# Performance work log

Hardware: AMD Instinct MI355X
Metric: run time of the kernel (lower is better)

The kernel has to match this reference:

```python
import jax, jax.numpy as jnp
import numpy as np

N = 256        # ImageSize
NC = 8         # coils
NSPOKE = 34    # radial spokes
NVEC = 512     # samples per spoke
K = NSPOKE * NVEC  # total k-space points


def setup_inputs() -> dict:
    key = jax.random.key(0)
    k1, k2, k3, k4 = jax.random.split(key, 4)
    input_r = jax.random.normal(k1, (N, N, 2), dtype=jnp.float32)
    C_r = jax.random.normal(k2, (NC, N, N, 2), dtype=jnp.float32)
    w = jax.random.uniform(k3, (NVEC,), dtype=jnp.float32)
    # nonuniform k-space coordinates in [-pi, pi)
    angle = jax.random.uniform(k4, (K, 2), dtype=jnp.float32,
                               minval=-np.pi, maxval=np.pi)
    return {"input_r": input_r, "C_r": C_r, "w": w, "angle": angle}


def reference(input_r, C_r, w, angle):
    # Type-3 NUFFT: y[c,k] = sum_j C[c,j]*x[j] * exp(-i*(s_k*(-x1_j) + t_k*(-x2_j)))
    #             = sum_{a,b} (C[c,a,b]*x[a,b]) * exp(+i*s_k*g[a]) * exp(+i*t_k*g[b])
    # since the source grid is separable: x1_j = g[a], x2_j = g[b],
    # g = linspace(-N//2, N//2-1, N) for even N (iflag=0 -> negative sign).
    n = input_r.shape[0]
    nvec = w.shape[0]
    g = jnp.arange(n, dtype=jnp.float32) - n // 2          # [N]

    x = input_r[..., 0] + 1j * input_r[..., 1]             # [N,N] complex64
    C = C_r[..., 0] + 1j * C_r[..., 1]                     # [Nc,N,N] complex64
    Xc = C * x[None]                                       # coil-weighted image [Nc,N,N]

    s = angle[:, 0]                                        # [K]
    t = angle[:, 1]                                        # [K]
    E1 = jnp.exp(1j * s[:, None] * g[None, :])             # [K,N] phase along axis a
    E2 = jnp.exp(1j * t[:, None] * g[None, :])             # [K,N] phase along axis b

    # contract b first -> [Nc,K,N], then a -> [Nc,K]
    y = jnp.einsum('kb,cab,ka->ck', E2, Xc, E1, optimize=True)  # [Nc,K]

    # density compensation: wr = tile(w, (Nc, Nspoke, 1)).reshape(Nc, -1)
    wr = jnp.tile(w, y.shape[1] // nvec)                   # [K]
    y = y * wr[None, :]

    return jnp.stack([jnp.real(y), jnp.imag(y)], axis=-1)  # [Nc,K,2] float32
```

## Files before the change

kernel.cpp:

```cpp
#include <hip/hip_runtime.h>
#include <hip/hip_bf16.h>
#include <stdint.h>


#define NKTOT 17408
#define NBLK 272
#define NT 8

typedef short bf16x8 __attribute__((ext_vector_type(8)));
typedef float f32x4 __attribute__((ext_vector_type(4)));

__device__ __forceinline__ unsigned short f2bf(float f) {
  unsigned int u = __builtin_bit_cast(unsigned int, f);
  u += 0x7FFFu + ((u >> 16) & 1u);
  return (unsigned short)(u >> 16);
}
__device__ __forceinline__ float bf2f(unsigned int lo16) {
  return __builtin_bit_cast(float, lo16 << 16);
}

__device__ __forceinline__ void async_copy16(void* lds, const void* g) {
  __builtin_amdgcn_global_load_lds(
      (const __attribute__((address_space(1))) unsigned int*)g,
      (__attribute__((address_space(3))) unsigned int*)lds, 16, 0, 0);
}

__device__ __forceinline__ size_t aidx(int c, int m, int jj) {
  int tt = jj >> 5;
  int s = ((m & 1) << 2) | ((jj >> 3) & 3);
  return (((size_t)(c * 8 + tt) * 256 + (m >> 1)) * 8 + s) * 8 + (jj & 7);
}
__device__ __forceinline__ size_t bidx(int kt, int kl, int jj) {
  int tt = jj >> 5;
  int s = ((kl & 1) << 2) | ((jj >> 3) & 3);
  return (((size_t)(kt * 8 + tt) * 32 + (kl >> 1)) * 8 + s) * 8 + (jj & 7);
}

__global__ __launch_bounds__(256) void pack_all(
    const float* __restrict__ input_r, const float* __restrict__ C_r,
    const float* __restrict__ angle,
    unsigned short* __restrict__ Apack, unsigned short* __restrict__ BT,
    float* __restrict__ biastab, unsigned int* __restrict__ E1tab)
{
  const int bx = blockIdx.x;
  const int tid = threadIdx.x;
  if (bx < 1024) {
    const int p = bx * 2 + (tid >> 7);
    const int a = p & 255;
    const int c = p >> 8;
    const int j = tid & 127;
    const size_t xbase = (size_t)a * 256;
    const size_t cbase = ((size_t)(c * 256 + a)) * 256;
    if (j == 0) {
      float xr = input_r[(xbase + 128) * 2], xi = input_r[(xbase + 128) * 2 + 1];
      float cr = C_r[(cbase + 128) * 2],     ci = C_r[(cbase + 128) * 2 + 1];
      biastab[c * 512 + a]       = cr * xr - ci * xi;
      biastab[c * 512 + 256 + a] = cr * xi + ci * xr;
      xr = input_r[xbase * 2]; xi = input_r[xbase * 2 + 1];
      cr = C_r[cbase * 2];     ci = C_r[cbase * 2 + 1];
      float reb = cr * xr - ci * xi, imb = cr * xi + ci * xr;
      Apack[aidx(c, a, 127)]       = f2bf(reb);
      Apack[aidx(c, a, 255)]       = f2bf(imb);
      Apack[aidx(c, 256 + a, 127)] = f2bf(imb);
      Apack[aidx(c, 256 + a, 255)] = f2bf(-reb);
    } else {
      const int bp = 128 + j, bm = 128 - j;
      float xpr = input_r[(xbase + bp) * 2], xpi = input_r[(xbase + bp) * 2 + 1];
      float cpr = C_r[(cbase + bp) * 2],     cpi = C_r[(cbase + bp) * 2 + 1];
      float pr = cpr * xpr - cpi * xpi, pi = cpr * xpi + cpi * xpr;
      float xmr = input_r[(xbase + bm) * 2], xmi = input_r[(xbase + bm) * 2 + 1];
      float cmr = C_r[(cbase + bm) * 2],     cmi = C_r[(cbase + bm) * 2 + 1];
      float mrv = cmr * xmr - cmi * xmi, miv = cmr * xmi + cmi * xmr;
      Apack[aidx(c, a, j - 1)]         = f2bf(pr + mrv);
      Apack[aidx(c, a, 127 + j)]       = f2bf(miv - pi);
      Apack[aidx(c, 256 + a, j - 1)]   = f2bf(pi + miv);
      Apack[aidx(c, 256 + a, 127 + j)] = f2bf(pr - mrv);
    }
  } else {
    const int k = bx - 1024;
    const int kt = k >> 6, kl = k & 63;
    const float s = angle[k * 2 + 0];
    const float t = angle[k * 2 + 1];
    float sn, cs;
    __sincosf(s * (float)(tid - 128), &sn, &cs);
    E1tab[(size_t)k * 256 + tid] =
        (unsigned int)f2bf(cs) | ((unsigned int)f2bf(sn) << 16);
    if (tid >= 1 && tid <= 128) {
      __sincosf(t * (float)tid, &sn, &cs);
      BT[bidx(kt, kl, tid - 1)]   = f2bf(cs);
      BT[bidx(kt, kl, 127 + tid)] = f2bf(sn);
    }
  }
}

__global__ __launch_bounds__(512, 4) void gemm_fused(
    const unsigned short* __restrict__ Apack,
    const unsigned short* __restrict__ BT,
    const float* __restrict__ biastab,
    const unsigned int* __restrict__ E1tab,
    const float* __restrict__ wvec,
    float* __restrict__ out)
{
  __shared__ unsigned short As[2][16384];
  __shared__ unsigned short Bs[2][2048];
  __shared__ float scol[8][2][64];

  const int bx = blockIdx.x;
  const int c = (bx >> 3) & 7;
  const int ktile = (bx >> 6) * 8 + (bx & 7);
  const int kt0 = ktile * 64;
  const int tid = threadIdx.x;
  const int w = tid >> 6;
  const int l = tid & 63;
  const int lhi = l >> 4;
  const int llo = l & 15;
  const int lr = l >> 3;
  const int lsw = ((l & 7) ^ lr) * 8;

  const unsigned short* Aimg = Apack + (size_t)c * (8 * 16384);
  const unsigned short* Bimg = BT + (size_t)ktile * (8 * 2048);
  const float* biasp = biastab + c * 512 + w * 64 + lhi * 4;

  const int u8 = ((((llo & 1) << 2) | lhi) ^ ((llo >> 1) & 7)) * 8;
  const int plbase = llo >> 1;

  f32x4 acc[4][4];
#pragma unroll
  for (int fi = 0; fi < 4; ++fi) {
    f32x4 b4 = *(const f32x4*)(biasp + fi * 16);
#pragma unroll
    for (int fj = 0; fj < 4; ++fj) acc[fi][fj] = b4;
  }

#pragma unroll
  for (int i = 0; i < 4; ++i) {
    int row0 = (w * 4 + i) * 8;
    async_copy16(&As[0][row0 * 64], Aimg + (size_t)(row0 + lr) * 64 + lsw);
  }
  if (w < 4)
    async_copy16(&Bs[0][w * 8 * 64], Bimg + (size_t)(w * 8 + lr) * 64 + lsw);
  __syncthreads();

#pragma unroll 2
  for (int tt = 0; tt < NT; ++tt) {
    const int cu = tt & 1;
    if (tt < NT - 1) {
      const unsigned short* Asrc = Aimg + (size_t)(tt + 1) * 16384;
      const unsigned short* Bsrc = Bimg + (size_t)(tt + 1) * 2048;
#pragma unroll
      for (int i = 0; i < 4; ++i) {
        int row0 = (w * 4 + i) * 8;
        async_copy16(&As[cu ^ 1][row0 * 64],
                     Asrc + (size_t)(row0 + lr) * 64 + lsw);
      }
      if (w < 4)
        async_copy16(&Bs[cu ^ 1][w * 8 * 64],
                     Bsrc + (size_t)(w * 8 + lr) * 64 + lsw);
    }
    __builtin_amdgcn_sched_barrier(0);

    bf16x8 bfr[4];
#pragma unroll
    for (int fj = 0; fj < 4; ++fj)
      bfr[fj] = *(const bf16x8*)&Bs[cu][(fj * 8 + plbase) * 64 + u8];
    bf16x8 af[4];
#pragma unroll
    for (int fi = 0; fi < 4; ++fi)
      af[fi] = *(const bf16x8*)&As[cu][(w * 32 + fi * 8 + plbase) * 64 + u8];
#pragma unroll
    for (int fi = 0; fi < 4; ++fi)
#pragma unroll
      for (int fj = 0; fj < 4; ++fj)
        acc[fi][fj] = __builtin_amdgcn_mfma_f32_16x16x32_bf16(
            af[fi], bfr[fj], acc[fi][fj], 0, 0, 0);
    __syncthreads();
  }

  const int aoff = (w & 3) * 64;
#pragma unroll
  for (int fj = 0; fj < 4; ++fj) {
    const int col = fj * 16 + llo;
    const int k = kt0 + col;
    float sumr = 0.f, sumi = 0.f;
    const unsigned int* e1base = E1tab + (size_t)k * 256 + aoff + lhi * 4;
#pragma unroll
    for (int fi = 0; fi < 4; ++fi) {
      uint4 e4 = *(const uint4*)(e1base + fi * 16);
      unsigned int ev[4] = {e4.x, e4.y, e4.z, e4.w};
#pragma unroll
      for (int r = 0; r < 4; ++r) {
        float v = acc[fi][fj][r];
        sumr += bf2f(ev[r] & 0xFFFFu) * v;
        sumi += bf2f(ev[r] >> 16) * v;
      }
    }
    sumr += __shfl_xor(sumr, 16, 64);
    sumr += __shfl_xor(sumr, 32, 64);
    sumi += __shfl_xor(sumi, 16, 64);
    sumi += __shfl_xor(sumi, 32, 64);
    if (lhi == 0) {
      scol[w][0][col] = sumr;
      scol[w][1][col] = sumi;
    }
  }
  __syncthreads();
  if (tid < 128) {
    const int col = tid >> 1;
    const int comp = tid & 1;
    const int k = kt0 + col;
    float re = scol[0][0][col] + scol[1][0][col] + scol[2][0][col] + scol[3][0][col]
             - scol[4][1][col] - scol[5][1][col] - scol[6][1][col] - scol[7][1][col];
    float im = scol[0][1][col] + scol[1][1][col] + scol[2][1][col] + scol[3][1][col]
             + scol[4][0][col] + scol[5][0][col] + scol[6][0][col] + scol[7][0][col];
    float val = comp ? im : re;
    out[((size_t)c * NKTOT + k) * 2 + comp] = val * wvec[k & 511];
  }
}

extern "C" void kernel_launch(void* const* d_in, const int* in_sizes, int n_in,
                              void* d_out, int out_size, void* d_ws, size_t ws_size,
                              hipStream_t stream) {
  const float* input_r = (const float*)d_in[0];
  const float* C_r     = (const float*)d_in[1];
  const float* wvec    = (const float*)d_in[2];
  const float* angle   = (const float*)d_in[3];
  float* out = (float*)d_out;

  unsigned short* Apack = (unsigned short*)d_ws;
  unsigned short* BT    = (unsigned short*)((char*)d_ws + (size_t)2097152);
  float*       biastab  = (float*)((char*)d_ws + (size_t)11010048);
  unsigned int* E1tab   = (unsigned int*)((char*)d_ws + (size_t)11026432);

  pack_all<<<1024 + NKTOT, 256, 0, stream>>>(input_r, C_r, angle,
                                             Apack, BT, biastab, E1tab);
  gemm_fused<<<8 * NBLK, 512, 0, stream>>>(Apack, BT, biastab, E1tab, wvec, out);
}
```

Baseline: 138.9 us.

## Compute B phase tiles and E1 phases on the fly inside the GEMM

Removes the precomputed BT and E1 tables. The GEMM now generates each B tile of cos/sin(t·j) directly into LDS while the MFMAs run, and builds the epilogue E1 phases from a single sincos through angle-doubling recurrences. This drops the large table writes and reads from global memory and shrinks the pack kernel to the A-side work only. In exchange, the GEMM does redundant transcendental work across the 8 coil blocks, and the fp32 recurrence can add small phase error.

Result: faster. 114.8 us (-17.3%).

```diff
diff --git a/kernel.cpp b/kernel.cpp
--- a/kernel.cpp
+++ b/kernel.cpp
@@ -15,9 +15,6 @@
   u += 0x7FFFu + ((u >> 16) & 1u);
   return (unsigned short)(u >> 16);
 }
-__device__ __forceinline__ float bf2f(unsigned int lo16) {
-  return __builtin_bit_cast(float, lo16 << 16);
-}
 
 __device__ __forceinline__ void async_copy16(void* lds, const void* g) {
   __builtin_amdgcn_global_load_lds(
@@ -30,74 +27,73 @@
   int s = ((m & 1) << 2) | ((jj >> 3) & 3);
   return (((size_t)(c * 8 + tt) * 256 + (m >> 1)) * 8 + s) * 8 + (jj & 7);
 }
-__device__ __forceinline__ size_t bidx(int kt, int kl, int jj) {
-  int tt = jj >> 5;
-  int s = ((kl & 1) << 2) | ((jj >> 3) & 3);
-  return (((size_t)(kt * 8 + tt) * 32 + (kl >> 1)) * 8 + s) * 8 + (jj & 7);
-}
-
-__global__ __launch_bounds__(256) void pack_all(
+
+__global__ __launch_bounds__(256) void pack_a(
     const float* __restrict__ input_r, const float* __restrict__ C_r,
-    const float* __restrict__ angle,
-    unsigned short* __restrict__ Apack, unsigned short* __restrict__ BT,
-    float* __restrict__ biastab, unsigned int* __restrict__ E1tab)
+    unsigned short* __restrict__ Apack, float* __restrict__ biastab)
 {
   const int bx = blockIdx.x;
   const int tid = threadIdx.x;
-  if (bx < 1024) {
-    const int p = bx * 2 + (tid >> 7);
-    const int a = p & 255;
-    const int c = p >> 8;
-    const int j = tid & 127;
-    const size_t xbase = (size_t)a * 256;
-    const size_t cbase = ((size_t)(c * 256 + a)) * 256;
-    if (j == 0) {
-      float xr = input_r[(xbase + 128) * 2], xi = input_r[(xbase + 128) * 2 + 1];
-      float cr = C_r[(cbase + 128) * 2],     ci = C_r[(cbase + 128) * 2 + 1];
-      biastab[c * 512 + a]       = cr * xr - ci * xi;
-      biastab[c * 512 + 256 + a] = cr * xi + ci * xr;
-      xr = input_r[xbase * 2]; xi = input_r[xbase * 2 + 1];
-      cr = C_r[cbase * 2];     ci = C_r[cbase * 2 + 1];
-      float reb = cr * xr - ci * xi, imb = cr * xi + ci * xr;
-      Apack[aidx(c, a, 127)]       = f2bf(reb);
-      Apack[aidx(c, a, 255)]       = f2bf(imb);
-      Apack[aidx(c, 256 + a, 127)] = f2bf(imb);
-      Apack[aidx(c, 256 + a, 255)] = f2bf(-reb);
-    } else {
-      const int bp = 128 + j, bm = 128 - j;
-      float xpr = input_r[(xbase + bp) * 2], xpi = input_r[(xbase + bp) * 2 + 1];
-      float cpr = C_r[(cbase + bp) * 2],     cpi = C_r[(cbase + bp) * 2 + 1];
-      float pr = cpr * xpr - cpi * xpi, pi = cpr * xpi + cpi * xpr;
-      float xmr = input_r[(xbase + bm) * 2], xmi = input_r[(xbase + bm) * 2 + 1];
-      float cmr = C_r[(cbase + bm) * 2],     cmi = C_r[(cbase + bm) * 2 + 1];
-      float mrv = cmr * xmr - cmi * xmi, miv = cmr * xmi + cmi * xmr;
-      Apack[aidx(c, a, j - 1)]         = f2bf(pr + mrv);
-      Apack[aidx(c, a, 127 + j)]       = f2bf(miv - pi);
-      Apack[aidx(c, 256 + a, j - 1)]   = f2bf(pi + miv);
-      Apack[aidx(c, 256 + a, 127 + j)] = f2bf(pr - mrv);
-    }
+  const int p = bx * 2 + (tid >> 7);
+  const int a = p & 255;
+  const int c = p >> 8;
+  const int j = tid & 127;
+  const size_t xbase = (size_t)a * 256;
+  const size_t cbase = ((size_t)(c * 256 + a)) * 256;
+  if (j == 0) {
+    float xr = input_r[(xbase + 128) * 2], xi = input_r[(xbase + 128) * 2 + 1];
+    float cr = C_r[(cbase + 128) * 2],     ci = C_r[(cbase + 128) * 2 + 1];
+    biastab[c * 512 + a]       = cr * xr - ci * xi;
+    biastab[c * 512 + 256 + a] = cr * xi + ci * xr;
+    xr = input_r[xbase * 2]; xi = input_r[xbase * 2 + 1];
+    cr = C_r[cbase * 2];     ci = C_r[cbase * 2 + 1];
+    float reb = cr * xr - ci * xi, imb = cr * xi + ci * xr;
+    Apack[aidx(c, a, 127)]       = f2bf(reb);
+    Apack[aidx(c, a, 255)]       = f2bf(imb);
+    Apack[aidx(c, 256 + a, 127)] = f2bf(imb);
+    Apack[aidx(c, 256 + a, 255)] = f2bf(-reb);
   } else {
-    const int k = bx - 1024;
-    const int kt = k >> 6, kl = k & 63;
-    const float s = angle[k * 2 + 0];
-    const float t = angle[k * 2 + 1];
-    float sn, cs;
-    __sincosf(s * (float)(tid - 128), &sn, &cs);
-    E1tab[(size_t)k * 256 + tid] =
-        (unsigned int)f2bf(cs) | ((unsigned int)f2bf(sn) << 16);
-    if (tid >= 1 && tid <= 128) {
-      __sincosf(t * (float)tid, &sn, &cs);
-      BT[bidx(kt, kl, tid - 1)]   = f2bf(cs);
-      BT[bidx(kt, kl, 127 + tid)] = f2bf(sn);
-    }
-  }
+    const int bp = 128 + j, bm = 128 - j;
+    float xpr = input_r[(xbase + bp) * 2], xpi = input_r[(xbase + bp) * 2 + 1];
+    float cpr = C_r[(cbase + bp) * 2],     cpi = C_r[(cbase + bp) * 2 + 1];
+    float pr = cpr * xpr - cpi * xpi, pi = cpr * xpi + cpi * xpr;
+    float xmr = input_r[(xbase + bm) * 2], xmi = input_r[(xbase + bm) * 2 + 1];
+    float cmr = C_r[(cbase + bm) * 2],     cmi = C_r[(cbase + bm) * 2 + 1];
+    float mrv = cmr * xmr - cmi * xmi, miv = cmr * xmi + cmi * xmr;
+    Apack[aidx(c, a, j - 1)]         = f2bf(pr + mrv);
+    Apack[aidx(c, a, 127 + j)]       = f2bf(miv - pi);
+    Apack[aidx(c, 256 + a, j - 1)]   = f2bf(pi + miv);
+    Apack[aidx(c, 256 + a, 127 + j)] = f2bf(pr - mrv);
+  }
+}
+
+__device__ __forceinline__ void b_compute(unsigned short* buf, float t,
+                                          int tile, int w, int l) {
+  const int p = l >> 1;
+  const int u = ((((l & 1) << 2) | (w >> 1)) ^ (p & 7));
+  const float jb = (float)((tile & 3) * 32 + w * 4 + 1);
+  float v0, v1, v2, v3;
+  if (tile < 4) {
+    v0 = __cosf(t * jb);
+    v1 = __cosf(t * (jb + 1.f));
+    v2 = __cosf(t * (jb + 2.f));
+    v3 = __cosf(t * (jb + 3.f));
+  } else {
+    v0 = __sinf(t * jb);
+    v1 = __sinf(t * (jb + 1.f));
+    v2 = __sinf(t * (jb + 2.f));
+    v3 = __sinf(t * (jb + 3.f));
+  }
+  uint2 pk;
+  pk.x = (unsigned int)f2bf(v0) | ((unsigned int)f2bf(v1) << 16);
+  pk.y = (unsigned int)f2bf(v2) | ((unsigned int)f2bf(v3) << 16);
+  *(uint2*)(buf + p * 64 + u * 8 + (w & 1) * 4) = pk;
 }
 
 __global__ __launch_bounds__(512, 4) void gemm_fused(
     const unsigned short* __restrict__ Apack,
-    const unsigned short* __restrict__ BT,
     const float* __restrict__ biastab,
-    const unsigned int* __restrict__ E1tab,
+    const float* __restrict__ angle,
     const float* __restrict__ wvec,
     float* __restrict__ out)
 {
@@ -118,11 +114,12 @@
   const int lsw = ((l & 7) ^ lr) * 8;
 
   const unsigned short* Aimg = Apack + (size_t)c * (8 * 16384);
-  const unsigned short* Bimg = BT + (size_t)ktile * (8 * 2048);
   const float* biasp = biastab + c * 512 + w * 64 + lhi * 4;
 
   const int u8 = ((((llo & 1) << 2) | lhi) ^ ((llo >> 1) & 7)) * 8;
   const int plbase = llo >> 1;
+
+  const float t_reg = angle[(size_t)(kt0 + l) * 2 + 1];
 
   f32x4 acc[4][4];
 #pragma unroll
@@ -137,8 +134,7 @@
     int row0 = (w * 4 + i) * 8;
     async_copy16(&As[0][row0 * 64], Aimg + (size_t)(row0 + lr) * 64 + lsw);
   }
-  if (w < 4)
-    async_copy16(&Bs[0][w * 8 * 64], Bimg + (size_t)(w * 8 + lr) * 64 + lsw);
+  b_compute(&Bs[0][0], t_reg, 0, w, l);
   __syncthreads();
 
 #pragma unroll 2
@@ -146,16 +142,12 @@
     const int cu = tt & 1;
     if (tt < NT - 1) {
       const unsigned short* Asrc = Aimg + (size_t)(tt + 1) * 16384;
-      const unsigned short* Bsrc = Bimg + (size_t)(tt + 1) * 2048;
 #pragma unroll
       for (int i = 0; i < 4; ++i) {
         int row0 = (w * 4 + i) * 8;
         async_copy16(&As[cu ^ 1][row0 * 64],
                      Asrc + (size_t)(row0 + lr) * 64 + lsw);
       }
-      if (w < 4)
-        async_copy16(&Bs[cu ^ 1][w * 8 * 64],
-                     Bsrc + (size_t)(w * 8 + lr) * 64 + lsw);
     }
     __builtin_amdgcn_sched_barrier(0);
 
@@ -173,27 +165,43 @@
       for (int fj = 0; fj < 4; ++fj)
         acc[fi][fj] = __builtin_amdgcn_mfma_f32_16x16x32_bf16(
             af[fi], bfr[fj], acc[fi][fj], 0, 0, 0);
+
+    if (tt < NT - 1) b_compute(&Bs[cu ^ 1][0], t_reg, tt + 1, w, l);
     __syncthreads();
   }
 
   const int aoff = (w & 3) * 64;
+  const float a0f = (float)(aoff + lhi * 4 - 128);
 #pragma unroll
   for (int fj = 0; fj < 4; ++fj) {
     const int col = fj * 16 + llo;
     const int k = kt0 + col;
-    float sumr = 0.f, sumi = 0.f;
-    const unsigned int* e1base = E1tab + (size_t)k * 256 + aoff + lhi * 4;
+    const float s = angle[(size_t)k * 2];
+    float s1, c1;
+    __sincosf(s, &s1, &c1);
+    float c2 = c1 * c1 - s1 * s1, s2 = 2.f * c1 * s1;
+    float c3 = c2 * c1 - s2 * s1, s3 = c2 * s1 + s2 * c1;
+    float c4 = c2 * c2 - s2 * s2,  s4 = 2.f * c2 * s2;
+    float c8 = c4 * c4 - s4 * s4,  s8 = 2.f * c4 * s4;
+    float cY = c8 * c8 - s8 * s8,  sY = 2.f * c8 * s8;
+    float cY2 = cY * cY - sY * sY, sY2 = 2.f * cY * sY;
+    float cY3 = cY2 * cY - sY2 * sY, sY3 = cY2 * sY + sY2 * cY;
+    const float Yr[4] = {1.f, cY, cY2, cY3};
+    const float Yi[4] = {0.f, sY, sY2, sY3};
+    float Or = 0.f, Oi = 0.f;
 #pragma unroll
     for (int fi = 0; fi < 4; ++fi) {
-      uint4 e4 = *(const uint4*)(e1base + fi * 16);
-      unsigned int ev[4] = {e4.x, e4.y, e4.z, e4.w};
-#pragma unroll
-      for (int r = 0; r < 4; ++r) {
-        float v = acc[fi][fj][r];
-        sumr += bf2f(ev[r] & 0xFFFFu) * v;
-        sumi += bf2f(ev[r] >> 16) * v;
-      }
+      float v0 = acc[fi][fj][0], v1 = acc[fi][fj][1];
+      float v2 = acc[fi][fj][2], v3 = acc[fi][fj][3];
+      float Ir = v0 + c1 * v1 + c2 * v2 + c3 * v3;
+      float Ii = s1 * v1 + s2 * v2 + s3 * v3;
+      Or += Yr[fi] * Ir - Yi[fi] * Ii;
+      Oi += Yi[fi] * Ir + Yr[fi] * Ii;
     }
+    float sb, cb;
+    __sincosf(s * a0f, &sb, &cb);
+    float sumr = cb * Or - sb * Oi;
+    float sumi = sb * Or + cb * Oi;
     sumr += __shfl_xor(sumr, 16, 64);
     sumr += __shfl_xor(sumr, 32, 64);
     sumi += __shfl_xor(sumi, 16, 64);
@@ -227,11 +235,8 @@
   float* out = (float*)d_out;
 
   unsigned short* Apack = (unsigned short*)d_ws;
-  unsigned short* BT    = (unsigned short*)((char*)d_ws + (size_t)2097152);
-  float*       biastab  = (float*)((char*)d_ws + (size_t)11010048);
-  unsigned int* E1tab   = (unsigned int*)((char*)d_ws + (size_t)11026432);
-
-  pack_all<<<1024 + NKTOT, 256, 0, stream>>>(input_r, C_r, angle,
-                                             Apack, BT, biastab, E1tab);
-  gemm_fused<<<8 * NBLK, 512, 0, stream>>>(Apack, BT, biastab, E1tab, wvec, out);
-}
+  float* biastab = (float*)((char*)d_ws + (size_t)2097152);
+
+  pack_a<<<1024, 256, 0, stream>>>(input_r, C_r, Apack, biastab);
+  gemm_fused<<<8 * NBLK, 512, 0, stream>>>(Apack, biastab, angle, wvec, out);
+}
```
